# Kernel tuning notes

Measured on AMD Instinct MI355X. Metric: run time of the kernel, lower is better.

Reference implementation:

```python
import jax, jax.numpy as jnp
import numpy as np

DIM = 2048
LAT = 512          # dim / compression_factor
NH = 16
NKV = 4
HD = LAT // NH     # 32
KVD = NKV * HD     # 128
K = 3              # conv kernel
GAIN = 0.25
EPS = 1e-6
THETA = 10000.0


def _rms(x, g):
    x32 = x.astype(jnp.float32)
    r = jax.lax.rsqrt(jnp.mean(x32 * x32, axis=-1, keepdims=True) + EPS)
    return (x32 * r).astype(x.dtype) * g.astype(x.dtype)


def _causal_conv(x, w, groups):
    # x: [B,S,C], w: [C, C//groups, K]; left-pad K-1 == pad both + trim right
    xc = jnp.transpose(x, (0, 2, 1))
    y = jax.lax.conv_general_dilated(
        xc, w, window_strides=(1,), padding=[(K - 1, 0)],
        feature_group_count=groups, dimension_numbers=('NCH', 'OIH', 'NCH'))
    return jnp.transpose(y, (0, 2, 1))


def _rope_tables(S):
    freqs = 1.0 / THETA ** (jnp.arange(0, HD, 2, dtype=jnp.float32) / HD)
    t = jnp.arange(S, dtype=jnp.float32)
    f = jnp.outer(t, freqs)               # [S, HD/2]
    return jnp.cos(f), jnp.sin(f)


def _rope(x, cos, sin):
    # x: [B,H,S,HD]; interleaved even/odd rotation
    x1, x2 = x[..., ::2], x[..., 1::2]
    r1 = x1 * cos - x2 * sin
    r2 = x1 * sin + x2 * cos
    return jnp.stack([r1, r2], axis=-1).reshape(x.shape)


def setup_inputs() -> dict:
    key = jax.random.key(0)
    ks = jax.random.split(key, 8)
    s = 0.02
    return {
        'x': jax.random.normal(ks[0], (4, 2048, DIM), jnp.float32),
        'w_q': jax.random.normal(ks[1], (LAT, DIM), jnp.float32) * s,
        'w_k': jax.random.normal(ks[2], (KVD, DIM), jnp.float32) * s,
        'w_v': jax.random.normal(ks[3], (KVD, DIM), jnp.float32) * s,
        'g_latent': jnp.ones((LAT,), jnp.float32),
        'g_kv': jnp.ones((KVD,), jnp.float32),
        'conv_q_w': jax.random.normal(ks[4], (LAT, LAT // NH, K), jnp.float32) * s,
        'conv_k_w': jax.random.normal(ks[5], (KVD, KVD // NKV, K), jnp.float32) * s,
        'g_conv': jnp.ones((LAT,), jnp.float32),
        'g_kconv': jnp.ones((KVD,), jnp.float32),
        'g_postq': jnp.ones((LAT,), jnp.float32),
        'g_postk': jnp.ones((KVD,), jnp.float32),
        'key_temp': jnp.ones((1,), jnp.float32),
        'g_preout': jnp.ones((LAT,), jnp.float32),
        'w_o': jax.random.normal(ks[6], (DIM, LAT), jnp.float32) * s,
    }


def reference(x, w_q, w_k, w_v, g_latent, g_kv, conv_q_w, conv_k_w,
              g_conv, g_kconv, g_postq, g_postk, key_temp, g_preout, w_o):
    B, S, D = x.shape
    n_groups = NH // NKV

    q = _rms(x @ w_q.T, g_latent)          # [B,S,LAT]
    k = _rms(x @ w_k.T, g_kv)              # [B,S,KVD]
    v = _rms(x @ w_v.T, g_kv)
    q_pre, k_pre = q, k

    q = _rms(_causal_conv(q, conv_q_w, NH), g_conv)
    k = _rms(_causal_conv(k, conv_k_w, NKV), g_kconv)

    # qk-mean modulation (n_groups > 1 branch)
    q_mean = q_pre.reshape(B, S, NH, HD).mean(axis=2)    # [B,S,HD]
    k_mean = k_pre.reshape(B, S, NKV, HD).mean(axis=2)   # [B,S,HD]
    q = q + GAIN * jnp.broadcast_to(k_mean[:, :, None, :], (B, S, NH, HD)).reshape(B, S, LAT)
    k = k + GAIN * jnp.broadcast_to(q_mean[:, :, None, :], (B, S, NKV, HD)).reshape(B, S, KVD)

    q = _rms(q, g_postq)
    k = _rms(k, g_postk)

    q = q.reshape(B, S, NH, HD).transpose(0, 2, 1, 3)    # [B,NH,S,HD]
    k = k.reshape(B, S, NKV, HD).transpose(0, 2, 1, 3)   # [B,NKV,S,HD]
    v = v.reshape(B, S, NKV, HD).transpose(0, 2, 1, 3)

    # QK L2 norm with learnable key temperature
    sqrt_hd = jnp.sqrt(jnp.float32(HD))
    qn = jnp.maximum(jnp.linalg.norm(q, axis=-1, keepdims=True), 1e-12)
    kn = jnp.maximum(jnp.linalg.norm(k, axis=-1, keepdims=True), 1e-12)
    q = q / qn * sqrt_hd
    k = k / kn * sqrt_hd * key_temp[0]

    cos, sin = _rope_tables(S)
    q = _rope(q, cos, sin)
    k = _rope(k, cos, sin)

    # GQA expand kv heads
    k = jnp.broadcast_to(k[:, :, None], (B, NKV, n_groups, S, HD)).reshape(B, NH, S, HD)
    v = jnp.broadcast_to(v[:, :, None], (B, NKV, n_groups, S, HD)).reshape(B, NH, S, HD)

    scale = HD ** -0.5
    scores = jnp.einsum('bhqd,bhkd->bhqk', q, k) * scale
    causal = jnp.tril(jnp.ones((S, S), bool))
    scores = jnp.where(causal, scores, jnp.finfo(scores.dtype).min)
    attn = jax.nn.softmax(scores, axis=-1)
    out = jnp.einsum('bhqk,bhkd->bhqd', attn, v)

    out = out.transpose(0, 2, 1, 3).reshape(B, S, LAT)
    out = _rms(out, g_preout)
    return out @ w_o.T
```

## Files before the change

### kernel.cpp

```cpp
#include <hip/hip_runtime.h>
#include <hip/hip_bf16.h>
#include <math.h>

constexpr int S_LEN = 2048;
constexpr int B_SZ  = 4;
constexpr int NROWS = B_SZ * S_LEN;
constexpr float GAIN_  = 0.25f;
constexpr float EPS_   = 1e-6f;
constexpr float THETA_ = 10000.0f;
constexpr float SCALE_ = 0.17677669529663687f;
constexpr float LOG2E_ = 1.44269504f;

typedef __attribute__((ext_vector_type(8))) short short8;
typedef __attribute__((ext_vector_type(4))) float float4v;

__device__ __forceinline__ short f2bs(float f) {
    __hip_bfloat16 h = __float2bfloat16(f);
    short r;
    __builtin_memcpy(&r, &h, 2);
    return r;
}

__device__ __forceinline__ void async_copy16(const short* g, short* l) {
    __builtin_amdgcn_global_load_lds(
        (const __attribute__((address_space(1))) void*)g,
        (__attribute__((address_space(3))) void*)l, 16, 0, 0);
}

__device__ __forceinline__ float block_reduce_sum_256(float v, float* scratch) {
    __syncthreads();
    for (int off = 32; off > 0; off >>= 1)
        v += __shfl_down(v, off, 64);
    int lane = threadIdx.x & 63;
    int wid  = threadIdx.x >> 6;
    if (lane == 0) scratch[wid] = v;
    __syncthreads();
    if (threadIdx.x == 0) scratch[0] = scratch[0] + scratch[1] + scratch[2] + scratch[3];
    __syncthreads();
    return scratch[0];
}

__global__ __launch_bounds__(256) void cvt_bf16(
    const float* __restrict__ src, short* __restrict__ dst, int n) {
    int i = (blockIdx.x * 256 + threadIdx.x) * 4;
    if (i >= n) return;
    float4 v = *(const float4*)(src + i);
    dst[i + 0] = f2bs(v.x); dst[i + 1] = f2bs(v.y);
    dst[i + 2] = f2bs(v.z); dst[i + 3] = f2bs(v.w);
}

__global__ __launch_bounds__(256) void cvt_weights(
    const float* __restrict__ wq, const float* __restrict__ wk,
    const float* __restrict__ wv, const float* __restrict__ wo,
    short* __restrict__ wqkvb, short* __restrict__ wob) {
    int i = (blockIdx.x * 256 + threadIdx.x) * 4;
    const float* src;
    short* dst;
    int j;
    if (i < 1048576)      { src = wq; dst = wqkvb + i; j = i; }
    else if (i < 1310720) { src = wk; dst = wqkvb + i; j = i - 1048576; }
    else if (i < 1572864) { src = wv; dst = wqkvb + i; j = i - 1310720; }
    else                  { src = wo; dst = wob + (i - 1572864); j = i - 1572864; }
    float4 v = *(const float4*)(src + j);
    dst[0] = f2bs(v.x); dst[1] = f2bs(v.y);
    dst[2] = f2bs(v.z); dst[3] = f2bs(v.w);
}

__global__ __launch_bounds__(256) void gemm_bf16_mfma(
    const short* __restrict__ A, const short* __restrict__ B,
    float* __restrict__ C, int N, int K) {
    __shared__ short As[128 * 32];
    __shared__ short Bs[128 * 32];
    int tid = threadIdx.x;
    int wave = tid >> 6, lane = tid & 63;
    int m0 = blockIdx.y * 128, n0 = blockIdx.x * 128;
    int wm = (wave >> 1) * 64, wn = (wave & 1) * 64;
    int mrow = lane & 15, quad = lane >> 4;
    float4v acc[4][4] = {};
    for (int k0 = 0; k0 < K; k0 += 32) {
        __syncthreads();
#pragma unroll
        for (int p = 0; p < 2; ++p) {
            int f = p * 256 + tid;
            int row = f >> 2, ch = (f & 3) * 8;
            const short* ga = A + (size_t)(m0 + row) * K + k0 + ch;
            const short* gb = B + (size_t)(n0 + row) * K + k0 + ch;
            async_copy16(ga, As + p * 2048 + wave * 512);
            async_copy16(gb, Bs + p * 2048 + wave * 512);
        }
        __syncthreads();
        short8 af[4], bf[4];
#pragma unroll
        for (int i = 0; i < 4; ++i)
            af[i] = *(const short8*)&As[(wm + i * 16 + mrow) * 32 + quad * 8];
#pragma unroll
        for (int j = 0; j < 4; ++j)
            bf[j] = *(const short8*)&Bs[(wn + j * 16 + mrow) * 32 + quad * 8];
#pragma unroll
        for (int i = 0; i < 4; ++i)
#pragma unroll
            for (int j = 0; j < 4; ++j)
                acc[i][j] = __builtin_amdgcn_mfma_f32_16x16x32_bf16(af[i], bf[j], acc[i][j], 0, 0, 0);
    }
#pragma unroll
    for (int i = 0; i < 4; ++i)
#pragma unroll
        for (int r = 0; r < 4; ++r) {
            int m = m0 + wm + i * 16 + quad * 4 + r;
            float* crow = C + (size_t)m * N + n0 + wn;
#pragma unroll
            for (int j = 0; j < 4; ++j)
                crow[j * 16 + mrow] = acc[i][j][r];
        }
}

__global__ __launch_bounds__(256) void rms_qkv_means(
    float* __restrict__ qkv, const float* __restrict__ g_latent,
    const float* __restrict__ g_kv,
    float* __restrict__ qmean, float* __restrict__ kmean,
    short* __restrict__ vtb) {
    int row = blockIdx.x;
    int b = row >> 11, s = row & (S_LEN - 1);
    float* p = qkv + (size_t)row * 768;
    __shared__ float sh[640];
    __shared__ float scratch[4];
    int tid = threadIdx.x;
    float v0 = p[tid], v1 = p[tid + 256], v2 = p[tid + 512];
    float ssq_q = block_reduce_sum_256(v0 * v0 + v1 * v1, scratch);
    float rq = rsqrtf(ssq_q / 512.f + EPS_);
    float q0 = v0 * rq * g_latent[tid];
    float q1 = v1 * rq * g_latent[tid + 256];
    p[tid] = q0; p[tid + 256] = q1;
    sh[tid] = q0; sh[tid + 256] = q1;
    float kpart = (tid < 128) ? v2 : 0.f;
    float vpart = (tid >= 128) ? v2 : 0.f;
    float ssq_k = block_reduce_sum_256(kpart * kpart, scratch);
    float ssq_v = block_reduce_sum_256(vpart * vpart, scratch);
    if (tid < 128) {
        float rk = rsqrtf(ssq_k / 128.f + EPS_);
        float kv = v2 * rk * g_kv[tid];
        p[512 + tid] = kv; sh[512 + tid] = kv;
    } else {
        float rv = rsqrtf(ssq_v / 128.f + EPS_);
        float vv = v2 * rv * g_kv[tid - 128];
        int d_full = tid - 128;
        vtb[((size_t)(b * 4 + (d_full >> 5)) * 32 + (d_full & 31)) * S_LEN + s] = f2bs(vv);
    }
    __syncthreads();
    if (tid < 32) {
        float sm = 0.f;
#pragma unroll
        for (int h = 0; h < 16; ++h) sm += sh[h * 32 + tid];
        qmean[(size_t)row * 32 + tid] = sm * (1.f / 16.f);
    } else if (tid < 64) {
        int d = tid - 32;
        float sm = 0.f;
#pragma unroll
        for (int h = 0; h < 4; ++h) sm += sh[512 + h * 32 + d];
        kmean[(size_t)row * 32 + d] = sm * 0.25f;
    }
}

__global__ __launch_bounds__(256) void causal_conv32(
    const float* __restrict__ in, int ldin, int inoff,
    const float* __restrict__ w, float* __restrict__ out, int C) {
    int b = blockIdx.z, g = blockIdx.y, s0 = blockIdx.x * 32;
    __shared__ float wsh[32][3][32];
    __shared__ float ish[34][33];
    int tid = threadIdx.x;
    for (int i = tid; i < 32 * 96; i += 256) {
        int oc = i / 96, r = i % 96;
        wsh[r / 3][r % 3][oc] = w[(size_t)(g * 32 + oc) * 96 + r];
    }
    for (int i = tid; i < 34 * 32; i += 256) {
        int pp = i >> 5, ic = i & 31;
        int s = s0 - 2 + pp;
        ish[pp][ic] = (s >= 0) ? in[((size_t)b * S_LEN + s) * ldin + inoff + g * 32 + ic] : 0.f;
    }
    __syncthreads();
    int sl = tid >> 3, oc0 = (tid & 7) * 4;
    float acc[4] = {0.f, 0.f, 0.f, 0.f};
    for (int ic = 0; ic < 32; ++ic) {
        float x0 = ish[sl][ic], x1 = ish[sl + 1][ic], x2 = ish[sl + 2][ic];
#pragma unroll
        for (int j = 0; j < 4; ++j)
            acc[j] += x0 * wsh[ic][0][oc0 + j] + x1 * wsh[ic][1][oc0 + j] + x2 * wsh[ic][2][oc0 + j];
    }
    float* orow = out + ((size_t)b * S_LEN + s0 + sl) * C + g * 32 + oc0;
    orow[0] = acc[0]; orow[1] = acc[1]; orow[2] = acc[2]; orow[3] = acc[3];
}

__global__ __launch_bounds__(256) void mix_rows(
    const float* __restrict__ convq, const float* __restrict__ convk,
    const float* __restrict__ qmean, const float* __restrict__ kmean,
    const float* __restrict__ g_conv, const float* __restrict__ g_kconv,
    const float* __restrict__ g_postq, const float* __restrict__ g_postk,
    const float* __restrict__ key_temp,
    short* __restrict__ qb, short* __restrict__ kb) {
    int row = blockIdx.x;
    int s = row & (S_LEN - 1);
    int tid = threadIdx.x;
    __shared__ float sh[640];
    __shared__ float scratch[4];
    __shared__ float hscale[20];
    float q0 = convq[(size_t)row * 512 + tid];
    float q1 = convq[(size_t)row * 512 + tid + 256];
    float k0 = (tid < 128) ? convk[(size_t)row * 128 + tid] : 0.f;
    float ssq = block_reduce_sum_256(q0 * q0 + q1 * q1, scratch);
    float r1 = rsqrtf(ssq / 512.f + EPS_);
    float ssk = block_reduce_sum_256(k0 * k0, scratch);
    float rk1 = rsqrtf(ssk / 128.f + EPS_);
    float km = kmean[(size_t)row * 32 + (tid & 31)];
    float a0 = q0 * r1 * g_conv[tid] + GAIN_ * km;
    float a1 = q1 * r1 * g_conv[tid + 256] + GAIN_ * km;
    float ak = 0.f;
    if (tid < 128) ak = k0 * rk1 * g_kconv[tid] + GAIN_ * qmean[(size_t)row * 32 + (tid & 31)];
    float ssq2 = block_reduce_sum_256(a0 * a0 + a1 * a1, scratch);
    float r2 = rsqrtf(ssq2 / 512.f + EPS_);
    float ssk2 = block_reduce_sum_256(ak * ak, scratch);
    float rk2 = rsqrtf(ssk2 / 128.f + EPS_);
    sh[tid] = a0 * r2 * g_postq[tid];
    sh[tid + 256] = a1 * r2 * g_postq[tid + 256];
    if (tid < 128) sh[512 + tid] = ak * rk2 * g_postk[tid];
    __syncthreads();
    if (tid < 16) {
        float ssh = 0.f;
        for (int d = 0; d < 32; ++d) { float x = sh[tid * 32 + d]; ssh += x * x; }
        hscale[tid] = 1.f / fmaxf(sqrtf(ssh), 1e-12f);
    } else if (tid < 20) {
        int h = tid - 16;
        float ssh = 0.f;
        for (int d = 0; d < 32; ++d) { float x = sh[512 + h * 32 + d]; ssh += x * x; }
        hscale[tid] = sqrtf(32.f) / fmaxf(sqrtf(ssh), 1e-12f) * key_temp[0];
    }
    __syncthreads();
    {
        int i0 = tid * 2;
        int h = i0 >> 5;
        int fi = (i0 & 31) >> 1;
        float sc = hscale[h];
        float x1 = sh[i0] * sc, x2 = sh[i0 + 1] * sc;
        float freq = powf(THETA_, -(float)fi / 16.f);
        float ang = (float)s * freq;
        float sn, cs;
        sincosf(ang, &sn, &cs);
        qb[(size_t)row * 512 + i0]     = f2bs(x1 * cs - x2 * sn);
        qb[(size_t)row * 512 + i0 + 1] = f2bs(x1 * sn + x2 * cs);
    }
    if (tid < 64) {
        int i0 = tid * 2;
        int h = i0 >> 5;
        int fi = (i0 & 31) >> 1;
        float sc = hscale[16 + h];
        float x1 = sh[512 + i0] * sc, x2 = sh[512 + i0 + 1] * sc;
        float freq = powf(THETA_, -(float)fi / 16.f);
        float ang = (float)s * freq;
        float sn, cs;
        sincosf(ang, &sn, &cs);
        kb[(size_t)row * 128 + i0]     = f2bs(x1 * cs - x2 * sn);
        kb[(size_t)row * 128 + i0 + 1] = f2bs(x1 * sn + x2 * cs);
    }
}

__global__ __launch_bounds__(256) void attn_mfma(
    const short* __restrict__ qb, const short* __restrict__ kb,
    const short* __restrict__ vtb, float* __restrict__ obuf,
    const float* __restrict__ key_temp) {
    int pair = blockIdx.x, h = blockIdx.y, b = blockIdx.z;
    int kvh = h >> 2;
    __shared__ short KF[2048];
    __shared__ short VF[2048];
    __shared__ __align__(16) short PF[4 * 16 * 72];
    int tid = threadIdx.x, wave = tid >> 6, lane = tid & 63;
    int cc = lane & 15, quad = lane >> 4;
    short* PFw = PF + wave * 16 * 72;
    float shift2 = -5.6568543f * key_temp[0] * LOG2E_;

    for (int half = 0; half < 2; ++half) {
        int qt = half ? (31 - pair) : pair;
        int s0 = qt * 64;
        short8 qfrag = *(const short8*)(qb +
            ((size_t)(b * S_LEN + s0 + wave * 16 + cc) * 512 + h * 32 + quad * 8));
        float4v accO[2];
        accO[0] = (float4v){0.f, 0.f, 0.f, 0.f};
        accO[1] = (float4v){0.f, 0.f, 0.f, 0.f};
        float lpart = 0.f;
        int qpos = s0 + wave * 16 + cc;

        for (int kt = 0; kt <= qt; ++kt) {
            __syncthreads();
            {
                int chunk = tid >> 6, q4 = (tid >> 4) & 3, c = tid & 15;
                const short* ksrc = kb +
                    ((size_t)(b * S_LEN + kt * 64 + chunk * 16 + c) * 128 + kvh * 32 + q4 * 8);
                async_copy16(ksrc, KF + chunk * 512);
                int kc = tid >> 7, dc = (tid >> 6) & 1;
                const short* vsrc = vtb +
                    ((size_t)((b * 4 + kvh) * 32 + dc * 16 + c) * S_LEN + kt * 64 + kc * 32 + q4 * 8);
                async_copy16(vsrc, VF + chunk * 512);
            }
            __syncthreads();

            float4v st[4];
#pragma unroll
            for (int chunk = 0; chunk < 4; ++chunk) {
                short8 kfrag = *(const short8*)&KF[chunk * 512 + lane * 8];
                float4v z = (float4v){0.f, 0.f, 0.f, 0.f};
                st[chunk] = __builtin_amdgcn_mfma_f32_16x16x32_bf16(kfrag, qfrag, z, 0, 0, 0);
            }

            bool diag = (kt == qt);
#pragma unroll
            for (int chunk = 0; chunk < 4; ++chunk) {
                float pv[4];
#pragma unroll
                for (int r = 0; r < 4; ++r) {
                    float e = exp2f(fmaf(st[chunk][r], LOG2E_, shift2));
                    if (diag) {
                        int kpos = kt * 64 + chunk * 16 + quad * 4 + r;
                        e = (kpos <= qpos) ? e : 0.f;
                    }
                    pv[r] = e;
                    lpart += e;
                }
                unsigned a0 = __float_as_uint(pv[0]) + 0x8000u;
                unsigned a1 = __float_as_uint(pv[1]) + 0x8000u;
                unsigned a2 = __float_as_uint(pv[2]) + 0x8000u;
                unsigned a3 = __float_as_uint(pv[3]) + 0x8000u;
                unsigned u0 = __builtin_amdgcn_perm(a1, a0, 0x07060302);
                unsigned u1 = __builtin_amdgcn_perm(a3, a2, 0x07060302);
                *(uint2*)&PFw[cc * 72 + chunk * 16 + quad * 4] = make_uint2(u0, u1);
            }

#pragma unroll
            for (int kc = 0; kc < 2; ++kc) {
                short8 pfrag = *(const short8*)&PFw[cc * 72 + kc * 32 + quad * 8];
#pragma unroll
                for (int dc = 0; dc < 2; ++dc) {
                    short8 vfrag = *(const short8*)&VF[(kc * 2 + dc) * 512 + lane * 8];
                    accO[dc] = __builtin_amdgcn_mfma_f32_16x16x32_bf16(pfrag, vfrag, accO[dc], 0, 0, 0);
                }
            }
        }

        lpart += __shfl_xor(lpart, 16, 64);
        lpart += __shfl_xor(lpart, 32, 64);
#pragma unroll
        for (int r = 0; r < 4; ++r) {
            float linv = 1.f / __shfl(lpart, quad * 4 + r, 64);
            float* dst = obuf +
                ((size_t)(b * S_LEN + s0 + wave * 16 + quad * 4 + r) * 512 + h * 32 + cc);
            dst[0]  = accO[0][r] * linv;
            dst[16] = accO[1][r] * linv;
        }
    }
}

__global__ __launch_bounds__(256) void rms_preout_bf16(
    const float* __restrict__ buf, const float* __restrict__ g,
    short* __restrict__ outb) {
    int row = blockIdx.x;
    const float* p = buf + (size_t)row * 512;
    __shared__ float scratch[4];
    int tid = threadIdx.x;
    float v0 = p[tid], v1 = p[tid + 256];
    float ssq = block_reduce_sum_256(v0 * v0 + v1 * v1, scratch);
    float r = rsqrtf(ssq / 512.f + EPS_);
    outb[(size_t)row * 512 + tid]       = f2bs(v0 * r * g[tid]);
    outb[(size_t)row * 512 + tid + 256] = f2bs(v1 * r * g[tid + 256]);
}

extern "C" void kernel_launch(void* const* d_in, const int* in_sizes, int n_in,
                              void* d_out, int out_size, void* d_ws, size_t ws_size,
                              hipStream_t stream) {
    (void)in_sizes; (void)n_in; (void)out_size; (void)ws_size;
    const float* x        = (const float*)d_in[0];
    const float* w_q      = (const float*)d_in[1];
    const float* w_k      = (const float*)d_in[2];
    const float* w_v      = (const float*)d_in[3];
    const float* g_latent = (const float*)d_in[4];
    const float* g_kv     = (const float*)d_in[5];
    const float* conv_q_w = (const float*)d_in[6];
    const float* conv_k_w = (const float*)d_in[7];
    const float* g_conv   = (const float*)d_in[8];
    const float* g_kconv  = (const float*)d_in[9];
    const float* g_postq  = (const float*)d_in[10];
    const float* g_postk  = (const float*)d_in[11];
    const float* key_temp = (const float*)d_in[12];
    const float* g_preout = (const float*)d_in[13];
    const float* w_o      = (const float*)d_in[14];
    float* out = (float*)d_out;

    char* ws = (char*)d_ws;
    const size_t R = NROWS;
    float* qkv   = (float*)ws;                        ws += R * 768 * 4;
    float* qmean = (float*)ws;                        ws += R * 32 * 4;
    float* kmean = (float*)ws;                        ws += R * 32 * 4;
    float* convq = (float*)ws;                        ws += R * 512 * 4;
    float* convk = (float*)ws;                        ws += R * 128 * 4;
    short* qbb   = (short*)ws;                        ws += R * 512 * 2;
    short* kbb   = (short*)ws;                        ws += R * 128 * 2;
    short* vtb   = (short*)ws;                        ws += R * 128 * 2;
    short* xb    = (short*)ws;                        ws += R * 2048 * 2;
    short* wqkvb = (short*)ws;                        ws += 768 * 2048 * 2;
    short* w_ob  = (short*)ws;                        ws += 2048 * 512 * 2;
    float* attn  = convq;
    short* attnb = xb;

    dim3 blk(256);
    cvt_bf16<<<(NROWS * 2048) / 1024, blk, 0, stream>>>(x, xb, NROWS * 2048);
    cvt_weights<<<2560, blk, 0, stream>>>(w_q, w_k, w_v, w_o, wqkvb, w_ob);

    gemm_bf16_mfma<<<dim3(6, 64), blk, 0, stream>>>(xb, wqkvb, qkv, 768, 2048);
    rms_qkv_means<<<NROWS, blk, 0, stream>>>(qkv, g_latent, g_kv, qmean, kmean, vtb);
    causal_conv32<<<dim3(64, 16, 4), blk, 0, stream>>>(qkv, 768, 0, conv_q_w, convq, 512);
    causal_conv32<<<dim3(64, 4, 4), blk, 0, stream>>>(qkv, 768, 512, conv_k_w, convk, 128);
    mix_rows<<<NROWS, blk, 0, stream>>>(convq, convk, qmean, kmean, g_conv, g_kconv,
                                        g_postq, g_postk, key_temp, qbb, kbb);
    attn_mfma<<<dim3(16, 16, 4), blk, 0, stream>>>(qbb, kbb, vtb, attn, key_temp);
    rms_preout_bf16<<<NROWS, blk, 0, stream>>>(attn, g_preout, attnb);
    gemm_bf16_mfma<<<dim3(16, 64), blk, 0, stream>>>(attnb, w_ob, out, 2048, 512);
}
```

Before: 400.3 us.

## Split attention key tiles across two blocks by parity and merge partials in RMS

Each attention block now handles only even or odd key tiles, which doubles the grid and halves the serial loop length per block. Each half writes unnormalized output numerators and row sums to separate buffers. The pre-output RMS kernel adds the two halves and divides by the summed denominator. This works because the softmax uses a fixed shift rather than a running max. The K/V load addresses are also hoisted and advanced incrementally. The cost is twice the fp32 intermediate traffic and extra reads in the RMS kernel, with partial buffers aliased onto existing workspace.

```diff
diff --git a/kernel.cpp b/kernel.cpp
--- a/kernel.cpp
+++ b/kernel.cpp
@@ -8,7 +8,6 @@
 constexpr float GAIN_  = 0.25f;
 constexpr float EPS_   = 1e-6f;
 constexpr float THETA_ = 10000.0f;
-constexpr float SCALE_ = 0.17677669529663687f;
 constexpr float LOG2E_ = 1.44269504f;
 
 typedef __attribute__((ext_vector_type(8))) short short8;
@@ -264,10 +263,14 @@
 
 __global__ __launch_bounds__(256) void attn_mfma(
     const short* __restrict__ qb, const short* __restrict__ kb,
-    const short* __restrict__ vtb, float* __restrict__ obuf,
-    const float* __restrict__ key_temp) {
-    int pair = blockIdx.x, h = blockIdx.y, b = blockIdx.z;
+    const short* __restrict__ vtb, float* __restrict__ OnumA,
+    float* __restrict__ OnumB, float* __restrict__ LsumA,
+    float* __restrict__ LsumB, const float* __restrict__ key_temp) {
+    int pp = blockIdx.x, h = blockIdx.y, b = blockIdx.z;
+    int pair = pp >> 1, parity = pp & 1;
     int kvh = h >> 2;
+    float* __restrict__ Onum = parity ? OnumB : OnumA;
+    float* __restrict__ Lsum = parity ? LsumB : LsumA;
     __shared__ short KF[2048];
     __shared__ short VF[2048];
     __shared__ __align__(16) short PF[4 * 16 * 72];
@@ -275,6 +278,13 @@
     int cc = lane & 15, quad = lane >> 4;
     short* PFw = PF + wave * 16 * 72;
     float shift2 = -5.6568543f * key_temp[0] * LOG2E_;
+
+    const short* ksrc0 = kb +
+        ((size_t)(b * S_LEN + parity * 64 + (tid >> 6) * 16 + (tid & 15)) * 128
+         + kvh * 32 + ((tid >> 4) & 3) * 8);
+    const short* vsrc0 = vtb +
+        ((size_t)((b * 4 + kvh) * 32 + ((tid >> 6) & 1) * 16 + (tid & 15)) * S_LEN
+         + parity * 64 + (tid >> 7) * 32 + ((tid >> 4) & 3) * 8);
 
     for (int half = 0; half < 2; ++half) {
         int qt = half ? (31 - pair) : pair;
@@ -286,19 +296,15 @@
         accO[1] = (float4v){0.f, 0.f, 0.f, 0.f};
         float lpart = 0.f;
         int qpos = s0 + wave * 16 + cc;
-
-        for (int kt = 0; kt <= qt; ++kt) {
+        const short* ksrc = ksrc0;
+        const short* vsrc = vsrc0;
+
+        for (int kt = parity; kt <= qt; kt += 2) {
             __syncthreads();
-            {
-                int chunk = tid >> 6, q4 = (tid >> 4) & 3, c = tid & 15;
-                const short* ksrc = kb +
-                    ((size_t)(b * S_LEN + kt * 64 + chunk * 16 + c) * 128 + kvh * 32 + q4 * 8);
-                async_copy16(ksrc, KF + chunk * 512);
-                int kc = tid >> 7, dc = (tid >> 6) & 1;
-                const short* vsrc = vtb +
-                    ((size_t)((b * 4 + kvh) * 32 + dc * 16 + c) * S_LEN + kt * 64 + kc * 32 + q4 * 8);
-                async_copy16(vsrc, VF + chunk * 512);
-            }
+            async_copy16(ksrc, KF + (tid >> 6) * 512);
+            async_copy16(vsrc, VF + (tid >> 6) * 512);
+            ksrc += 2 * 64 * 128;
+            vsrc += 2 * 64;
             __syncthreads();
 
             float4v st[4];
@@ -345,25 +351,32 @@
 
         lpart += __shfl_xor(lpart, 16, 64);
         lpart += __shfl_xor(lpart, 32, 64);
+        if (quad == 0)
+            Lsum[((size_t)(b * S_LEN + s0 + wave * 16 + cc)) * 16 + h] = lpart;
 #pragma unroll
         for (int r = 0; r < 4; ++r) {
-            float linv = 1.f / __shfl(lpart, quad * 4 + r, 64);
-            float* dst = obuf +
+            float* dst = Onum +
                 ((size_t)(b * S_LEN + s0 + wave * 16 + quad * 4 + r) * 512 + h * 32 + cc);
-            dst[0]  = accO[0][r] * linv;
-            dst[16] = accO[1][r] * linv;
+            dst[0]  = accO[0][r];
+            dst[16] = accO[1][r];
         }
     }
 }
 
 __global__ __launch_bounds__(256) void rms_preout_bf16(
-    const float* __restrict__ buf, const float* __restrict__ g,
-    short* __restrict__ outb) {
+    const float* __restrict__ OA, const float* __restrict__ OB,
+    const float* __restrict__ LA, const float* __restrict__ LB,
+    const float* __restrict__ g, short* __restrict__ outb) {
     int row = blockIdx.x;
-    const float* p = buf + (size_t)row * 512;
     __shared__ float scratch[4];
+    __shared__ float linv[16];
     int tid = threadIdx.x;
-    float v0 = p[tid], v1 = p[tid + 256];
+    if (tid < 16)
+        linv[tid] = 1.f / (LA[(size_t)row * 16 + tid] + LB[(size_t)row * 16 + tid]);
+    __syncthreads();
+    float v0 = (OA[(size_t)row * 512 + tid] + OB[(size_t)row * 512 + tid]) * linv[tid >> 5];
+    float v1 = (OA[(size_t)row * 512 + tid + 256] + OB[(size_t)row * 512 + tid + 256])
+               * linv[(tid + 256) >> 5];
     float ssq = block_reduce_sum_256(v0 * v0 + v1 * v1, scratch);
     float r = rsqrtf(ssq / 512.f + EPS_);
     outb[(size_t)row * 512 + tid]       = f2bs(v0 * r * g[tid]);
@@ -404,7 +417,10 @@
     short* xb    = (short*)ws;                        ws += R * 2048 * 2;
     short* wqkvb = (short*)ws;                        ws += 768 * 2048 * 2;
     short* w_ob  = (short*)ws;                        ws += 2048 * 512 * 2;
-    float* attn  = convq;
+    float* OnumA = convq;
+    float* OnumB = qkv;
+    float* LsumA = qmean;
+    float* LsumB = kmean;
     short* attnb = xb;
 
     dim3 blk(256);
@@ -417,7 +433,9 @@
     causal_conv32<<<dim3(64, 4, 4), blk, 0, stream>>>(qkv, 768, 512, conv_k_w, convk, 128);
     mix_rows<<<NROWS, blk, 0, stream>>>(convq, convk, qmean, kmean, g_conv, g_kconv,
                                         g_postq, g_postk, key_temp, qbb, kbb);
-    attn_mfma<<<dim3(16, 16, 4), blk, 0, stream>>>(qbb, kbb, vtb, attn, key_temp);
-    rms_preout_bf16<<<NROWS, blk, 0, stream>>>(attn, g_preout, attnb);
+    attn_mfma<<<dim3(32, 16, 4), blk, 0, stream>>>(qbb, kbb, vtb, OnumA, OnumB,
+                                                   LsumA, LsumB, key_temp);
+    rms_preout_bf16<<<NROWS, blk, 0, stream>>>(OnumA, OnumB, LsumA, LsumB,
+                                               g_preout, attnb);
     gemm_bf16_mfma<<<dim3(16, 64), blk, 0, stream>>>(attnb, w_ob, out, 2048, 512);
 }
```

Result: no change. 398.8 us (-0.4%).
